# Optimization experiments

Hardware: AMD Instinct MI355X
Metric: run time of the kernel (lower is better)

## Reference

```python
import jax, jax.numpy as jnp
import numpy as np

N = 131072
D = 512        # input_dim
H = 512        # hidden_dim
E = 10         # num_experts
INIT_STD_SCALE = 0.1


def _trunc_normal(key, shape, std):
    # approximate trunc_normal_(std=std) in [-2std, 2std]
    return jnp.clip(jax.random.normal(key, shape) * std, -2.0 * std, 2.0 * std).astype(jnp.float32)


def setup_inputs() -> dict:
    key = jax.random.key(0)
    ks = jax.random.split(key, 6)
    x = jax.random.normal(ks[0], (N, D), dtype=jnp.float32)
    # router (default nn.Linear init approximated with uniform)
    lim = 1.0 / np.sqrt(D)
    Wr = jax.random.uniform(ks[1], (E, D), minval=-lim, maxval=lim, dtype=jnp.float32)
    br = jnp.zeros((E,), dtype=jnp.float32)
    # experts: trunc_normal with std = 0.1 / sqrt(fan_in), zero bias
    W1 = _trunc_normal(ks[2], (E, D, H), INIT_STD_SCALE / np.sqrt(D))   # [E, D, H]
    b1 = jnp.zeros((E, H), dtype=jnp.float32)
    W2 = _trunc_normal(ks[3], (E, H, H), INIT_STD_SCALE / np.sqrt(H))   # [E, H, H]
    b2 = jnp.zeros((E, H), dtype=jnp.float32)
    return {"x": x, "Wr": Wr, "br": br, "W1": W1, "b1": b1, "W2": W2, "b2": b2}


def reference(x, Wr, br, W1, b1, W2, b2):
    # router in fp32 (autocast disabled in original)
    logits = x.astype(jnp.float32) @ Wr.T + br          # [N, E]
    expert_ids = jnp.argmax(logits, axis=1)              # [N]
    out = jnp.zeros((x.shape[0], W2.shape[-1]), dtype=x.dtype)
    # fixed small loop over experts; dropout is identity at inference
    for e in range(W1.shape[0]):
        h = jax.nn.relu(x @ W1[e] + b1[e])                # [N, H]
        o = h @ W2[e] + b2[e]                             # [N, H]
        out = jnp.where((expert_ids == e)[:, None], o, out)
    return out, expert_ids
```

## Files before the change

kernel.cpp:

```cpp
#include <hip/hip_runtime.h>
#include <hip/hip_bf16.h>

#define N_TOK 131072
#define DIM   512
#define HID   512
#define NEXP  10

using bf16x8 = __attribute__((ext_vector_type(8))) short;
using f32x4  = __attribute__((ext_vector_type(4))) float;

__device__ __forceinline__ short f2bf(float f) {
    union { float f; unsigned u; } v; v.f = f;
    unsigned u = v.u;
    return (short)((u + 0x7FFFu + ((u >> 16) & 1u)) >> 16);
}

#define GLOAD16(g, l) __builtin_amdgcn_global_load_lds( \
    (const __attribute__((address_space(1))) void*)(g),  \
    (__attribute__((address_space(3))) void*)(l), 16, 0, 0)

__global__ __launch_bounds__(256) void router_kernel(
    const float* __restrict__ x, const float* __restrict__ Wr,
    const float* __restrict__ br, int* __restrict__ eid,
    float* __restrict__ ids_out, int* __restrict__ counts,
    short* __restrict__ xb)
{
    __shared__ float wr[NEXP][DIM];
    __shared__ int lcnt[NEXP];
    int tid = threadIdx.x;
    for (int i = tid; i < NEXP * DIM / 4; i += 256)
        ((float4*)wr)[i] = ((const float4*)Wr)[i];
    if (tid < NEXP) lcnt[tid] = 0;
    __syncthreads();

    int lane  = tid & 63;
    int wave  = tid >> 6;
    int gwave = blockIdx.x * 4 + wave;
    int nwav  = gridDim.x * 4;

    for (int t = gwave; t < N_TOK; t += nwav) {
        const float4* xr = (const float4*)(x + (size_t)t * DIM);
        float4 v0 = xr[lane * 2], v1 = xr[lane * 2 + 1];
        float xf[8] = {v0.x, v0.y, v0.z, v0.w, v1.x, v1.y, v1.z, v1.w};
        bf16x8 p;
        #pragma unroll
        for (int j = 0; j < 8; ++j) p[j] = f2bf(xf[j]);
        *(bf16x8*)(xb + (size_t)t * DIM + lane * 8) = p;

        float dot[NEXP];
        #pragma unroll
        for (int e = 0; e < NEXP; ++e) {
            const float* wv = &wr[e][lane * 8];
            float s = 0.f;
            #pragma unroll
            for (int j = 0; j < 8; ++j) s = fmaf(xf[j], wv[j], s);
            dot[e] = s;
        }
        #pragma unroll
        for (int off = 32; off > 0; off >>= 1) {
            #pragma unroll
            for (int e = 0; e < NEXP; ++e) dot[e] += __shfl_xor(dot[e], off, 64);
        }
        if (lane == 0) {
            int best = 0; float bv = dot[0] + br[0];
            #pragma unroll
            for (int e = 1; e < NEXP; ++e) {
                float v = dot[e] + br[e];
                if (v > bv) { bv = v; best = e; }
            }
            eid[t] = best;
            ids_out[t] = (float)best;
            atomicAdd(&lcnt[best], 1);
        }
    }
    __syncthreads();
    if (tid < NEXP) atomicAdd(&counts[tid], lcnt[tid]);
}

__global__ void offsets_kernel(const int* __restrict__ counts,
                               int* __restrict__ offsets, int* __restrict__ toff)
{
    if (threadIdx.x == 0) {
        int acc = 0, ta = 0;
        for (int e = 0; e < NEXP; ++e) {
            offsets[e] = acc; toff[e] = ta;
            acc += counts[e]; ta += (counts[e] + 127) >> 7;
        }
        offsets[NEXP] = acc; toff[NEXP] = ta;
    }
}

__global__ __launch_bounds__(256) void scatter_kernel(
    const int* __restrict__ eid, const int* __restrict__ offsets,
    int* __restrict__ cursors, int* __restrict__ perm)
{
    __shared__ int lcnt[NEXP], lbase[NEXP];
    int tid = threadIdx.x;
    if (tid < NEXP) lcnt[tid] = 0;
    __syncthreads();
    int t = blockIdx.x * 256 + tid;
    int e = 0, lpos = 0;
    if (t < N_TOK) {
        e = eid[t];
        lpos = atomicAdd(&lcnt[e], 1);
    }
    __syncthreads();
    if (tid < NEXP) lbase[tid] = atomicAdd(&cursors[tid], lcnt[tid]);
    __syncthreads();
    if (t < N_TOK) perm[offsets[e] + lbase[e] + lpos] = t;
}

__global__ __launch_bounds__(256) void wconvert_kernel(
    const float* __restrict__ W1, const float* __restrict__ W2,
    short* __restrict__ W1b, short* __restrict__ W2b)
{
    int mat = blockIdx.z;
    const float* src = (mat < NEXP) ? W1 + (size_t)mat * 512 * 512
                                    : W2 + (size_t)(mat - NEXP) * 512 * 512;
    short* dst = (mat < NEXP) ? W1b + (size_t)mat * 512 * 512
                              : W2b + (size_t)(mat - NEXP) * 512 * 512;
    __shared__ float tile[64][65];
    int r0 = blockIdx.y * 64, c0 = blockIdx.x * 64;
    int tid = threadIdx.x;
    int tr = tid >> 4, tc4 = (tid & 15) * 4;
    #pragma unroll
    for (int i = 0; i < 4; ++i) {
        float4 v = *(const float4*)(src + (size_t)(r0 + i * 16 + tr) * 512 + c0 + tc4);
        tile[i * 16 + tr][tc4 + 0] = v.x; tile[i * 16 + tr][tc4 + 1] = v.y;
        tile[i * 16 + tr][tc4 + 2] = v.z; tile[i * 16 + tr][tc4 + 3] = v.w;
    }
    __syncthreads();
    int s   = (r0 + tc4) >> 5;
    int kin = (r0 + tc4) & 31;
    #pragma unroll
    for (int i = 0; i < 4; ++i) {
        int cc = i * 16 + tr;
        ushort4 o;
        o.x = (ushort)f2bf(tile[tc4 + 0][cc]); o.y = (ushort)f2bf(tile[tc4 + 1][cc]);
        o.z = (ushort)f2bf(tile[tc4 + 2][cc]); o.w = (ushort)f2bf(tile[tc4 + 3][cc]);
        *(ushort4*)(dst + (size_t)s * 16384 + (size_t)(c0 + cc) * 32 + kin) = o;
    }
}

template<int LAYER>
__global__ __launch_bounds__(256, 3) void expert_gemm(
    const short* __restrict__ xb, const short* __restrict__ hA,
    const short* __restrict__ WT, const float* __restrict__ bias,
    const int* __restrict__ offsets, const int* __restrict__ toff,
    const int* __restrict__ perm,
    short* __restrict__ hOut, float* __restrict__ out)
{
    int g = blockIdx.x;
    if (g >= toff[NEXP]) return;
    int e = 0;
    #pragma unroll
    for (int k = 1; k < NEXP; ++k) e += (g >= toff[k]);
    int beg = offsets[e], cnt = offsets[e + 1] - beg;
    int m0 = (g - toff[e]) * 128;
    int nb = blockIdx.y * 128;

    __shared__ int toks[128];
    __shared__ short Ab[3][128 * 32];
    __shared__ short Bb[3][128 * 32];

    int tid = threadIdx.x, lane = tid & 63, w = tid >> 6;
    if (tid < 128) toks[tid] = perm[beg + min(m0 + tid, cnt - 1)];
    __syncthreads();

    const short* WTe = WT + (size_t)e * 512 * 512;
    const short* aSrc[2];
    const short* bSrc[2];
    #pragma unroll
    for (int k = 0; k < 2; ++k) {
        int s   = w * 128 + k * 64 + lane;
        int row = s >> 2;
        int ql  = (s & 3) ^ ((row >> 1) & 3);
        bSrc[k] = WTe + (size_t)(nb + row) * 32 + ql * 8;
        if (LAYER == 1) aSrc[k] = xb + (size_t)toks[row] * DIM + ql * 8;
        else            aSrc[k] = hA + (size_t)(beg + min(m0 + row, cnt - 1)) * HID + ql * 8;
    }

    auto stage = [&](int t, int b) {
        #pragma unroll
        for (int k = 0; k < 2; ++k) {
            GLOAD16(aSrc[k] + t * 32,    (char*)&Ab[b][0] + w * 2048 + k * 1024);
            GLOAD16(bSrc[k] + t * 16384, (char*)&Bb[b][0] + w * 2048 + k * 1024);
        }
    };

    int wr = w >> 1, wc = w & 1, lrow = lane & 15, kq = lane >> 4;
    int offA[4], offB[4];
    #pragma unroll
    for (int i = 0; i < 4; ++i) {
        int r = wr * 64 + i * 16 + lrow;
        offA[i] = r * 64 + (kq ^ ((r >> 1) & 3)) * 16;
    }
    #pragma unroll
    for (int j = 0; j < 4; ++j) {
        int r = wc * 64 + j * 16 + lrow;
        offB[j] = r * 64 + (kq ^ ((r >> 1) & 3)) * 16;
    }

    f32x4 acc[4][4];
    #pragma unroll
    for (int i = 0; i < 4; ++i)
        #pragma unroll
        for (int j = 0; j < 4; ++j) acc[i][j] = (f32x4){0.f, 0.f, 0.f, 0.f};

    auto comp = [&](int b) {
        bf16x8 af[4], bv[4];
        #pragma unroll
        for (int i = 0; i < 4; ++i) af[i] = *(const bf16x8*)((char*)&Ab[b][0] + offA[i]);
        #pragma unroll
        for (int j = 0; j < 4; ++j) bv[j] = *(const bf16x8*)((char*)&Bb[b][0] + offB[j]);
        __builtin_amdgcn_s_setprio(1);
        #pragma unroll
        for (int i = 0; i < 4; ++i)
            #pragma unroll
            for (int j = 0; j < 4; ++j)
                acc[i][j] = __builtin_amdgcn_mfma_f32_16x16x32_bf16(af[i], bv[j], acc[i][j], 0, 0, 0);
        __builtin_amdgcn_s_setprio(0);
    };

    stage(0, 0);
    stage(1, 1);
    asm volatile("s_waitcnt vmcnt(4)" ::: "memory");
    __builtin_amdgcn_s_barrier();

    #pragma unroll
    for (int t = 0; t < 16; ++t) {
        if (t + 2 < 16) stage(t + 2, (t + 2) % 3);
        comp(t % 3);
        if (t == 15) break;
        if (t + 2 < 16) asm volatile("s_waitcnt vmcnt(4)" ::: "memory");
        else            asm volatile("s_waitcnt vmcnt(0)" ::: "memory");
        __builtin_amdgcn_s_barrier();
    }

    const float* be = bias + (size_t)e * 512;
    int colb = nb + wc * 64 + lrow;
    float bvv[4];
    #pragma unroll
    for (int j = 0; j < 4; ++j) bvv[j] = be[colb + j * 16];

    #pragma unroll
    for (int i = 0; i < 4; ++i) {
        #pragma unroll
        for (int q = 0; q < 4; ++q) {
            int rr = wr * 64 + i * 16 + kq * 4 + q;
            if (m0 + rr < cnt) {
                if (LAYER == 1) {
                    short* hp = hOut + (size_t)(beg + m0 + rr) * HID + colb;
                    #pragma unroll
                    for (int j = 0; j < 4; ++j) {
                        float v = acc[i][j][q] + bvv[j];
                        hp[j * 16] = f2bf(v > 0.f ? v : 0.f);
                    }
                } else {
                    float* op = out + (size_t)toks[rr] * HID + colb;
                    #pragma unroll
                    for (int j = 0; j < 4; ++j)
                        op[j * 16] = acc[i][j][q] + bvv[j];
                }
            }
        }
    }
}

extern "C" void kernel_launch(void* const* d_in, const int* in_sizes, int n_in,
                              void* d_out, int out_size, void* d_ws, size_t ws_size,
                              hipStream_t stream)
{
    const float* x  = (const float*)d_in[0];
    const float* Wr = (const float*)d_in[1];
    const float* br = (const float*)d_in[2];
    const float* W1 = (const float*)d_in[3];
    const float* b1 = (const float*)d_in[4];
    const float* W2 = (const float*)d_in[5];
    const float* b2 = (const float*)d_in[6];

    float* out     = (float*)d_out;
    float* ids_out = out + (size_t)N_TOK * HID;

    char* ws     = (char*)d_ws;
    int* counts  = (int*)ws;
    int* offsets = counts + 16;
    int* toff    = counts + 32;
    int* cursors = counts + 48;
    int* eid     = (int*)(ws + 1024);
    int* perm    = eid + N_TOK;
    short* W1b   = (short*)(ws + 1024 + (size_t)2 * N_TOK * 4);
    short* W2b   = W1b + (size_t)NEXP * 512 * 512;
    short* h     = W2b + (size_t)NEXP * 512 * 512;
    short* xb    = h   + (size_t)N_TOK * HID;

    hipMemsetAsync(d_ws, 0, 1024, stream);
    router_kernel<<<2048, 256, 0, stream>>>(x, Wr, br, eid, ids_out, counts, xb);
    wconvert_kernel<<<dim3(8, 8, 2 * NEXP), 256, 0, stream>>>(W1, W2, W1b, W2b);
    offsets_kernel<<<1, 64, 0, stream>>>(counts, offsets, toff);
    scatter_kernel<<<512, 256, 0, stream>>>(eid, offsets, cursors, perm);

    int ntiles = (N_TOK + 127) / 128 + NEXP;
    expert_gemm<1><<<dim3(ntiles, 4), 256, 0, stream>>>(xb, nullptr, W1b, b1, offsets, toff, perm, h, nullptr);
    expert_gemm<2><<<dim3(ntiles, 4), 256, 0, stream>>>(nullptr, h, W2b, b2, offsets, toff, perm, nullptr, out);
}
```

Baseline: 408.0 us.

## Replace LDS-staged triple-buffered GEMM with direct global-to-register MFMA loads

Removes the shared-memory staging (global_load_lds triple buffering and barriers) from the expert GEMM; each wave now loads A and B fragments straight from global memory into registers. The tile shape changes from 128x128 to 64 rows by 256 columns: all four waves share the same 64 token rows and each owns 64 columns, and the offsets kernel now counts 64-row tiles. This drops barrier and LDS traffic but loses cross-wave reuse through LDS and the explicit load/compute overlap, so it leans on cache hits and the compiler to hide global latency.

```diff
diff --git a/kernel.cpp b/kernel.cpp
--- a/kernel.cpp
+++ b/kernel.cpp
@@ -14,10 +14,6 @@
     unsigned u = v.u;
     return (short)((u + 0x7FFFu + ((u >> 16) & 1u)) >> 16);
 }
-
-#define GLOAD16(g, l) __builtin_amdgcn_global_load_lds( \
-    (const __attribute__((address_space(1))) void*)(g),  \
-    (__attribute__((address_space(3))) void*)(l), 16, 0, 0)
 
 __global__ __launch_bounds__(256) void router_kernel(
     const float* __restrict__ x, const float* __restrict__ Wr,
@@ -84,7 +80,7 @@
         int acc = 0, ta = 0;
         for (int e = 0; e < NEXP; ++e) {
             offsets[e] = acc; toff[e] = ta;
-            acc += counts[e]; ta += (counts[e] + 127) >> 7;
+            acc += counts[e]; ta += (counts[e] + 63) >> 6;
         }
         offsets[NEXP] = acc; toff[NEXP] = ta;
     }
@@ -156,49 +152,26 @@
     #pragma unroll
     for (int k = 1; k < NEXP; ++k) e += (g >= toff[k]);
     int beg = offsets[e], cnt = offsets[e + 1] - beg;
-    int m0 = (g - toff[e]) * 128;
-    int nb = blockIdx.y * 128;
-
-    __shared__ int toks[128];
-    __shared__ short Ab[3][128 * 32];
-    __shared__ short Bb[3][128 * 32];
-
-    int tid = threadIdx.x, lane = tid & 63, w = tid >> 6;
-    if (tid < 128) toks[tid] = perm[beg + min(m0 + tid, cnt - 1)];
-    __syncthreads();
+    int m0 = (g - toff[e]) * 64;
+    int nb = blockIdx.y * 256;
+
+    int tid = threadIdx.x, lane = tid & 63, wq = tid >> 6;
+    int lrow = lane & 15, kq = lane >> 4;
 
     const short* WTe = WT + (size_t)e * 512 * 512;
-    const short* aSrc[2];
-    const short* bSrc[2];
-    #pragma unroll
-    for (int k = 0; k < 2; ++k) {
-        int s   = w * 128 + k * 64 + lane;
-        int row = s >> 2;
-        int ql  = (s & 3) ^ ((row >> 1) & 3);
-        bSrc[k] = WTe + (size_t)(nb + row) * 32 + ql * 8;
-        if (LAYER == 1) aSrc[k] = xb + (size_t)toks[row] * DIM + ql * 8;
-        else            aSrc[k] = hA + (size_t)(beg + min(m0 + row, cnt - 1)) * HID + ql * 8;
-    }
-
-    auto stage = [&](int t, int b) {
-        #pragma unroll
-        for (int k = 0; k < 2; ++k) {
-            GLOAD16(aSrc[k] + t * 32,    (char*)&Ab[b][0] + w * 2048 + k * 1024);
-            GLOAD16(bSrc[k] + t * 16384, (char*)&Bb[b][0] + w * 2048 + k * 1024);
-        }
-    };
-
-    int wr = w >> 1, wc = w & 1, lrow = lane & 15, kq = lane >> 4;
-    int offA[4], offB[4];
-    #pragma unroll
-    for (int i = 0; i < 4; ++i) {
-        int r = wr * 64 + i * 16 + lrow;
-        offA[i] = r * 64 + (kq ^ ((r >> 1) & 3)) * 16;
-    }
+
+    const short* aP[4];
+    #pragma unroll
+    for (int i = 0; i < 4; ++i) {
+        int r = min(m0 + i * 16 + lrow, cnt - 1);
+        if (LAYER == 1) aP[i] = xb + (size_t)perm[beg + r] * DIM + kq * 8;
+        else            aP[i] = hA + (size_t)(beg + r) * HID + kq * 8;
+    }
+    const short* bP[4];
     #pragma unroll
     for (int j = 0; j < 4; ++j) {
-        int r = wc * 64 + j * 16 + lrow;
-        offB[j] = r * 64 + (kq ^ ((r >> 1) & 3)) * 16;
+        int c = nb + wq * 64 + j * 16 + lrow;
+        bP[j] = WTe + (size_t)c * 32 + kq * 8;
     }
 
     f32x4 acc[4][4];
@@ -207,38 +180,22 @@
         #pragma unroll
         for (int j = 0; j < 4; ++j) acc[i][j] = (f32x4){0.f, 0.f, 0.f, 0.f};
 
-    auto comp = [&](int b) {
+    #pragma unroll 4
+    for (int t = 0; t < 16; ++t) {
         bf16x8 af[4], bv[4];
         #pragma unroll
-        for (int i = 0; i < 4; ++i) af[i] = *(const bf16x8*)((char*)&Ab[b][0] + offA[i]);
-        #pragma unroll
-        for (int j = 0; j < 4; ++j) bv[j] = *(const bf16x8*)((char*)&Bb[b][0] + offB[j]);
-        __builtin_amdgcn_s_setprio(1);
+        for (int i = 0; i < 4; ++i) af[i] = *(const bf16x8*)(aP[i] + t * 32);
+        #pragma unroll
+        for (int j = 0; j < 4; ++j) bv[j] = *(const bf16x8*)(bP[j] + (size_t)t * 16384);
         #pragma unroll
         for (int i = 0; i < 4; ++i)
             #pragma unroll
             for (int j = 0; j < 4; ++j)
                 acc[i][j] = __builtin_amdgcn_mfma_f32_16x16x32_bf16(af[i], bv[j], acc[i][j], 0, 0, 0);
-        __builtin_amdgcn_s_setprio(0);
-    };
-
-    stage(0, 0);
-    stage(1, 1);
-    asm volatile("s_waitcnt vmcnt(4)" ::: "memory");
-    __builtin_amdgcn_s_barrier();
-
-    #pragma unroll
-    for (int t = 0; t < 16; ++t) {
-        if (t + 2 < 16) stage(t + 2, (t + 2) % 3);
-        comp(t % 3);
-        if (t == 15) break;
-        if (t + 2 < 16) asm volatile("s_waitcnt vmcnt(4)" ::: "memory");
-        else            asm volatile("s_waitcnt vmcnt(0)" ::: "memory");
-        __builtin_amdgcn_s_barrier();
     }
 
     const float* be = bias + (size_t)e * 512;
-    int colb = nb + wc * 64 + lrow;
+    int colb = nb + wq * 64 + lrow;
     float bvv[4];
     #pragma unroll
     for (int j = 0; j < 4; ++j) bvv[j] = be[colb + j * 16];
@@ -247,7 +204,7 @@
     for (int i = 0; i < 4; ++i) {
         #pragma unroll
         for (int q = 0; q < 4; ++q) {
-            int rr = wr * 64 + i * 16 + kq * 4 + q;
+            int rr = i * 16 + kq * 4 + q;
             if (m0 + rr < cnt) {
                 if (LAYER == 1) {
                     short* hp = hOut + (size_t)(beg + m0 + rr) * HID + colb;
@@ -257,7 +214,7 @@
                         hp[j * 16] = f2bf(v > 0.f ? v : 0.f);
                     }
                 } else {
-                    float* op = out + (size_t)toks[rr] * HID + colb;
+                    float* op = out + (size_t)perm[beg + m0 + rr] * HID + colb;
                     #pragma unroll
                     for (int j = 0; j < 4; ++j)
                         op[j * 16] = acc[i][j][q] + bvv[j];
@@ -300,7 +257,7 @@
     offsets_kernel<<<1, 64, 0, stream>>>(counts, offsets, toff);
     scatter_kernel<<<512, 256, 0, stream>>>(eid, offsets, cursors, perm);
 
-    int ntiles = (N_TOK + 127) / 128 + NEXP;
-    expert_gemm<1><<<dim3(ntiles, 4), 256, 0, stream>>>(xb, nullptr, W1b, b1, offsets, toff, perm, h, nullptr);
-    expert_gemm<2><<<dim3(ntiles, 4), 256, 0, stream>>>(nullptr, h, W2b, b2, offsets, toff, perm, nullptr, out);
-}
+    int ntiles = (N_TOK + 63) / 64 + NEXP;
+    expert_gemm<1><<<dim3(ntiles, 2), 256, 0, stream>>>(xb, nullptr, W1b, b1, offsets, toff, perm, h, nullptr);
+    expert_gemm<2><<<dim3(ntiles, 2), 256, 0, stream>>>(nullptr, h, W2b, b2, offsets, toff, perm, nullptr, out);
+}
```

Measured after the change: 586.5 us. 43.8% more time.

## Use 512-thread blocks covering 256 columns, looping two halves per tile

Applied to the files above, without the earlier changes.

The expert GEMM now uses 8 waves per block, each block computing a 128x256 output slab and looping over two column halves, so the full 512 columns of a token tile come from one block instead of four. This cuts the number of blocks that gather the same A rows and uses a larger shared-memory buffer for A and B staging. Layer 1 output is written through shared memory as coalesced 16-byte rows instead of scattered 2-byte stores. In exchange, shared-memory use per block rises to about 72 KB, which limits occupancy, and each block does more serial work.

```diff
diff --git a/kernel.cpp b/kernel.cpp
--- a/kernel.cpp
+++ b/kernel.cpp
@@ -143,7 +143,7 @@
 }
 
 template<int LAYER>
-__global__ __launch_bounds__(256, 3) void expert_gemm(
+__global__ __launch_bounds__(512, 4) void expert_gemm(
     const short* __restrict__ xb, const short* __restrict__ hA,
     const short* __restrict__ WT, const float* __restrict__ bias,
     const int* __restrict__ offsets, const int* __restrict__ toff,
@@ -157,38 +157,31 @@
     for (int k = 1; k < NEXP; ++k) e += (g >= toff[k]);
     int beg = offsets[e], cnt = offsets[e + 1] - beg;
     int m0 = (g - toff[e]) * 128;
-    int nb = blockIdx.y * 128;
 
     __shared__ int toks[128];
-    __shared__ short Ab[3][128 * 32];
-    __shared__ short Bb[3][128 * 32];
+    __shared__ char SMEM[73728];
 
     int tid = threadIdx.x, lane = tid & 63, w = tid >> 6;
     if (tid < 128) toks[tid] = perm[beg + min(m0 + tid, cnt - 1)];
     __syncthreads();
 
     const short* WTe = WT + (size_t)e * 512 * 512;
-    const short* aSrc[2];
-    const short* bSrc[2];
-    #pragma unroll
-    for (int k = 0; k < 2; ++k) {
-        int s   = w * 128 + k * 64 + lane;
-        int row = s >> 2;
-        int ql  = (s & 3) ^ ((row >> 1) & 3);
-        bSrc[k] = WTe + (size_t)(nb + row) * 32 + ql * 8;
-        if (LAYER == 1) aSrc[k] = xb + (size_t)toks[row] * DIM + ql * 8;
-        else            aSrc[k] = hA + (size_t)(beg + min(m0 + row, cnt - 1)) * HID + ql * 8;
-    }
-
-    auto stage = [&](int t, int b) {
-        #pragma unroll
-        for (int k = 0; k < 2; ++k) {
-            GLOAD16(aSrc[k] + t * 32,    (char*)&Ab[b][0] + w * 2048 + k * 1024);
-            GLOAD16(bSrc[k] + t * 16384, (char*)&Bb[b][0] + w * 2048 + k * 1024);
-        }
+    int srow = w * 16 + (lane >> 2);
+    int kqp  = lane & 3;
+    int ql   = kqp ^ ((srow >> 1) & 3);
+    const short* aS;
+    if (LAYER == 1) aS = xb + (size_t)toks[srow] * DIM + ql * 8;
+    else            aS = hA + (size_t)(beg + min(m0 + srow, cnt - 1)) * HID + ql * 8;
+    const short* bS = WTe + (size_t)srow * 32 + ql * 8;
+
+    auto stage = [&](int t, int b, int nb) {
+        const short* bs = bS + nb * 32 + t * 16384;
+        GLOAD16(bs,            SMEM + 24576 + b * 16384 + tid * 16);
+        GLOAD16(bs + 4096,     SMEM + 24576 + b * 16384 + 8192 + tid * 16);
+        GLOAD16(aS + t * 32,   SMEM + b * 8192 + tid * 16);
     };
 
-    int wr = w >> 1, wc = w & 1, lrow = lane & 15, kq = lane >> 4;
+    int wr = w >> 2, wc = w & 3, lrow = lane & 15, kq = lane >> 4;
     int offA[4], offB[4];
     #pragma unroll
     for (int i = 0; i < 4; ++i) {
@@ -201,68 +194,93 @@
         offB[j] = r * 64 + (kq ^ ((r >> 1) & 3)) * 16;
     }
 
-    f32x4 acc[4][4];
-    #pragma unroll
-    for (int i = 0; i < 4; ++i)
-        #pragma unroll
-        for (int j = 0; j < 4; ++j) acc[i][j] = (f32x4){0.f, 0.f, 0.f, 0.f};
-
-    auto comp = [&](int b) {
-        bf16x8 af[4], bv[4];
-        #pragma unroll
-        for (int i = 0; i < 4; ++i) af[i] = *(const bf16x8*)((char*)&Ab[b][0] + offA[i]);
-        #pragma unroll
-        for (int j = 0; j < 4; ++j) bv[j] = *(const bf16x8*)((char*)&Bb[b][0] + offB[j]);
-        __builtin_amdgcn_s_setprio(1);
+    const float* be = bias + (size_t)e * 512;
+
+    #pragma unroll 1
+    for (int half = 0; half < 2; ++half) {
+        int nb = half * 256;
+
+        f32x4 acc[4][4];
         #pragma unroll
         for (int i = 0; i < 4; ++i)
             #pragma unroll
+            for (int j = 0; j < 4; ++j) acc[i][j] = (f32x4){0.f, 0.f, 0.f, 0.f};
+
+        auto comp = [&](int b) {
+            bf16x8 af[4], bv[4];
+            #pragma unroll
+            for (int i = 0; i < 4; ++i)
+                af[i] = *(const bf16x8*)(SMEM + b * 8192 + offA[i]);
+            #pragma unroll
             for (int j = 0; j < 4; ++j)
-                acc[i][j] = __builtin_amdgcn_mfma_f32_16x16x32_bf16(af[i], bv[j], acc[i][j], 0, 0, 0);
-        __builtin_amdgcn_s_setprio(0);
-    };
-
-    stage(0, 0);
-    stage(1, 1);
-    asm volatile("s_waitcnt vmcnt(4)" ::: "memory");
-    __builtin_amdgcn_s_barrier();
-
-    #pragma unroll
-    for (int t = 0; t < 16; ++t) {
-        if (t + 2 < 16) stage(t + 2, (t + 2) % 3);
-        comp(t % 3);
-        if (t == 15) break;
-        if (t + 2 < 16) asm volatile("s_waitcnt vmcnt(4)" ::: "memory");
-        else            asm volatile("s_waitcnt vmcnt(0)" ::: "memory");
+                bv[j] = *(const bf16x8*)(SMEM + 24576 + b * 16384 + offB[j]);
+            __builtin_amdgcn_s_setprio(1);
+            #pragma unroll
+            for (int i = 0; i < 4; ++i)
+                #pragma unroll
+                for (int j = 0; j < 4; ++j)
+                    acc[i][j] = __builtin_amdgcn_mfma_f32_16x16x32_bf16(af[i], bv[j], acc[i][j], 0, 0, 0);
+            __builtin_amdgcn_s_setprio(0);
+        };
+
+        stage(0, 0, nb);
+        stage(1, 1, nb);
+        asm volatile("s_waitcnt vmcnt(3)" ::: "memory");
         __builtin_amdgcn_s_barrier();
-    }
-
-    const float* be = bias + (size_t)e * 512;
-    int colb = nb + wc * 64 + lrow;
-    float bvv[4];
-    #pragma unroll
-    for (int j = 0; j < 4; ++j) bvv[j] = be[colb + j * 16];
-
-    #pragma unroll
-    for (int i = 0; i < 4; ++i) {
-        #pragma unroll
-        for (int q = 0; q < 4; ++q) {
-            int rr = wr * 64 + i * 16 + kq * 4 + q;
-            if (m0 + rr < cnt) {
-                if (LAYER == 1) {
-                    short* hp = hOut + (size_t)(beg + m0 + rr) * HID + colb;
+
+        #pragma unroll
+        for (int t = 0; t < 16; ++t) {
+            if (t + 2 < 16) stage(t + 2, (t + 2) % 3, nb);
+            comp(t % 3);
+            if (t == 15) break;
+            if (t + 2 < 16) asm volatile("s_waitcnt vmcnt(3)" ::: "memory");
+            else            asm volatile("s_waitcnt vmcnt(0)" ::: "memory");
+            __builtin_amdgcn_s_barrier();
+        }
+        __builtin_amdgcn_s_barrier();
+
+        int colb = nb + wc * 64 + lrow;
+        float bvv[4];
+        #pragma unroll
+        for (int j = 0; j < 4; ++j) bvv[j] = be[colb + j * 16];
+
+        if (LAYER == 1) {
+            #pragma unroll
+            for (int i = 0; i < 4; ++i)
+                #pragma unroll
+                for (int q = 0; q < 4; ++q) {
+                    int rr = wr * 64 + i * 16 + kq * 4 + q;
                     #pragma unroll
                     for (int j = 0; j < 4; ++j) {
+                        int c = wc * 64 + j * 16 + lrow;
                         float v = acc[i][j][q] + bvv[j];
-                        hp[j * 16] = f2bf(v > 0.f ? v : 0.f);
+                        *(short*)(SMEM + rr * 528 + c * 2) = f2bf(v > 0.f ? v : 0.f);
                     }
-                } else {
-                    float* op = out + (size_t)toks[rr] * HID + colb;
-                    #pragma unroll
-                    for (int j = 0; j < 4; ++j)
-                        op[j * 16] = acc[i][j][q] + bvv[j];
+                }
+            __syncthreads();
+            int ch = tid & 31, rg = tid >> 5;
+            #pragma unroll
+            for (int s = 0; s < 8; ++s) {
+                int row = rg * 8 + s;
+                if (m0 + row < cnt) {
+                    bf16x8 vv = *(const bf16x8*)(SMEM + row * 528 + ch * 16);
+                    *(bf16x8*)(hOut + (size_t)(beg + m0 + row) * HID + nb + ch * 8) = vv;
                 }
             }
+            __syncthreads();
+        } else {
+            #pragma unroll
+            for (int i = 0; i < 4; ++i)
+                #pragma unroll
+                for (int q = 0; q < 4; ++q) {
+                    int rr = wr * 64 + i * 16 + kq * 4 + q;
+                    if (m0 + rr < cnt) {
+                        float* op = out + (size_t)toks[rr] * HID + colb;
+                        #pragma unroll
+                        for (int j = 0; j < 4; ++j)
+                            op[j * 16] = acc[i][j][q] + bvv[j];
+                    }
+                }
         }
     }
 }
@@ -301,6 +319,6 @@
     scatter_kernel<<<512, 256, 0, stream>>>(eid, offsets, cursors, perm);
 
     int ntiles = (N_TOK + 127) / 128 + NEXP;
-    expert_gemm<1><<<dim3(ntiles, 4), 256, 0, stream>>>(xb, nullptr, W1b, b1, offsets, toff, perm, h, nullptr);
-    expert_gemm<2><<<dim3(ntiles, 4), 256, 0, stream>>>(nullptr, h, W2b, b2, offsets, toff, perm, nullptr, out);
-}
+    expert_gemm<1><<<ntiles, 512, 0, stream>>>(xb, nullptr, W1b, b1, offsets, toff, perm, h, nullptr);
+    expert_gemm<2><<<ntiles, 512, 0, stream>>>(nullptr, h, W2b, b2, offsets, toff, perm, nullptr, out);
+}
```

Measured after the change: 497.6 us. +22.0%, slower.
